# Optimization experiments

Measured on AMD Instinct MI355X. Metric: run time of the kernel, lower is better.

## Reference

```python
import jax, jax.numpy as jnp
import numpy as np

B, S, D, H, DFF = 2, 2048, 1024, 16, 4096
DH = D // H
EPS = 1e-5


def setup_inputs() -> dict:
    key = jax.random.key(0)
    ks = jax.random.split(key, 12)
    s = 0.02
    x = jax.random.normal(ks[0], (B, S, D), dtype=jnp.float32)
    # causal decoder mask, True = keep
    mask = jnp.tril(jnp.ones((S, S), dtype=bool))[None, None, :, :]
    Wq = jax.random.normal(ks[1], (D, D), dtype=jnp.float32) * s
    Wk = jax.random.normal(ks[2], (D, D), dtype=jnp.float32) * s
    Wv = jax.random.normal(ks[3], (D, D), dtype=jnp.float32) * s
    Wo = jax.random.normal(ks[4], (D, D), dtype=jnp.float32) * s
    w1 = jax.random.normal(ks[5], (D, DFF), dtype=jnp.float32) * s
    b1 = jnp.zeros((DFF,), dtype=jnp.float32)
    w2 = jax.random.normal(ks[6], (DFF, D), dtype=jnp.float32) * s
    b2 = jnp.zeros((D,), dtype=jnp.float32)
    g1 = jnp.ones((D,), dtype=jnp.float32)
    be1 = jnp.zeros((D,), dtype=jnp.float32)
    g2 = jnp.ones((D,), dtype=jnp.float32)
    be2 = jnp.zeros((D,), dtype=jnp.float32)
    return dict(x=x, mask=mask, Wq=Wq, Wk=Wk, Wv=Wv, Wo=Wo,
                w1=w1, b1=b1, w2=w2, b2=b2, g1=g1, be1=be1, g2=g2, be2=be2)


def _layer_norm(x, gamma, beta):
    mu = jnp.mean(x, axis=-1, keepdims=True)
    var = jnp.mean(jnp.square(x - mu), axis=-1, keepdims=True)
    return (x - mu) * jax.lax.rsqrt(var + EPS) * gamma + beta


def _attention(x, mask, Wq, Wk, Wv, Wo):
    # x: [B,S,D] -> q,k,v: [B,H,S,DH]
    def split_heads(t):
        return t.reshape(x.shape[0], x.shape[1], H, DH).transpose(0, 2, 1, 3)
    q = split_heads(x @ Wq)
    k = split_heads(x @ Wk)
    v = split_heads(x @ Wv)
    scores = jnp.einsum('bhqd,bhkd->bhqk', q, k) / jnp.sqrt(jnp.float32(DH))
    scores = jnp.where(mask, scores, jnp.float32(-1e9))
    probs = jax.nn.softmax(scores, axis=-1)
    out = jnp.einsum('bhqk,bhkd->bhqd', probs, v)  # [B,H,S,DH]
    out = out.transpose(0, 2, 1, 3).reshape(x.shape[0], x.shape[1], -1)
    return out @ Wo


def reference(x, mask, Wq, Wk, Wv, Wo, w1, b1, w2, b2, g1, be1, g2, be2):
    # residual 1: pre-norm self-attention (dropout=0)
    h = x + _attention(_layer_norm(x, g1, be1), mask, Wq, Wk, Wv, Wo)
    # residual 2: pre-norm FFN
    hn = _layer_norm(h, g2, be2)
    ffn = jax.nn.relu(hn @ w1 + b1) @ w2 + b2
    return h + ffn
```

## Files before the change

kernel.cpp:

```cpp
#include <hip/hip_runtime.h>

typedef unsigned short u16;
typedef __attribute__((ext_vector_type(8))) short short8;
typedef __attribute__((ext_vector_type(4))) float f32x4;

#define CB 2
#define CS 2048
#define CD 1024
#define CH 16
#define CDH 64
#define CDFF 4096
#define NQB (CS / 64)

__device__ __forceinline__ u16 f2bf(float f){
  union { float f; unsigned u; } x; x.f = f;
  unsigned r = (x.u + 0x7fffu + ((x.u >> 16) & 1u)) >> 16;
  return (u16)r;
}

__device__ __forceinline__ u16 f2bf_pos(float f){
  union { float f; unsigned u; } x; x.f = f;
  return (u16)((x.u + 0x8000u) >> 16);
}

__device__ __forceinline__ void gload_lds16(const void* g, void* l){
  __builtin_amdgcn_global_load_lds(
    (const __attribute__((address_space(1))) void*)(unsigned long long)g,
    (__attribute__((address_space(3))) void*)(unsigned long long)l,
    16, 0, 0);
}


struct TPAll { const float* s[6]; u16* d[6]; };

__global__ __launch_bounds__(256)
void prep_all(TPAll p, const float* __restrict__ x, const float* __restrict__ g1,
              const float* __restrict__ be1, u16* __restrict__ yln)
{
  const int g = blockIdx.x >> 12;
  const int id = blockIdx.x & 4095;
  const int tid = threadIdx.x;

  if (g == 3){
    const int row = id;
    const int lane = tid & 63, wave = tid >> 6;
    const float4 v = ((const float4*)(x + (size_t)row * CD))[tid];
    float s  = v.x + v.y + v.z + v.w;
    float s2 = v.x*v.x + v.y*v.y + v.z*v.z + v.w*v.w;
    #pragma unroll
    for (int m = 1; m < 64; m <<= 1){ s += __shfl_xor(s, m); s2 += __shfl_xor(s2, m); }
    __shared__ float red[8];
    if (lane == 0){ red[wave] = s; red[4 + wave] = s2; }
    __syncthreads();
    s  = red[0] + red[1] + red[2] + red[3];
    s2 = red[4] + red[5] + red[6] + red[7];
    const float mu = s * (1.0f / CD);
    const float var = s2 * (1.0f / CD) - mu * mu;
    const float rs = rsqrtf(var + 1e-5f);
    const float4 gv = ((const float4*)g1)[tid];
    const float4 bv = ((const float4*)be1)[tid];
    ushort4 o;
    o.x = f2bf((v.x - mu) * rs * gv.x + bv.x);
    o.y = f2bf((v.y - mu) * rs * gv.y + bv.y);
    o.z = f2bf((v.z - mu) * rs * gv.z + bv.z);
    o.w = f2bf((v.w - mu) * rs * gv.w + bv.w);
    ((ushort4*)yln)[(size_t)row * (CD / 4) + tid] = o;
    return;
  }

  __shared__ float t[32][33];
  const float* __restrict__ in;
  u16* __restrict__ out;
  int K, N, n0, k0;
  if (g == 0){
    const int w = id >> 10, tile = id & 1023;
    in = p.s[w]; out = p.d[w]; K = 1024; N = 1024;
    n0 = (tile & 31) * 32; k0 = (tile >> 5) * 32;
  } else if (g == 1){
    in = p.s[4]; out = p.d[4]; K = 1024; N = 4096;
    n0 = (id & 127) * 32; k0 = (id >> 7) * 32;
  } else {
    in = p.s[5]; out = p.d[5]; K = 4096; N = 1024;
    n0 = (id & 31) * 32; k0 = (id >> 5) * 32;
  }
  const int c = tid & 31, r4 = tid >> 5;
  #pragma unroll
  for (int i = 0; i < 4; i++){
    int r = r4 + i * 8;
    t[r][c] = in[(size_t)(k0 + r) * N + n0 + c];
  }
  __syncthreads();
  #pragma unroll
  for (int i = 0; i < 4; i++){
    int r = r4 + i * 8;
    out[(size_t)(n0 + r) * K + k0 + c] = f2bf(t[c][r]);
  }
}

template<int MODE>
__global__ __launch_bounds__(256)
void ln_bf16(const float* __restrict__ xin, const float* __restrict__ g,
             const float* __restrict__ be, u16* __restrict__ outp,
             float4* __restrict__ aux, const float* __restrict__ bias)
{
  const int row = blockIdx.x, tid = threadIdx.x;
  const int lane = tid & 63, wave = tid >> 6;
  const float4 v = ((const float4*)(xin + (size_t)row * CD))[tid];
  float s  = v.x + v.y + v.z + v.w;
  float s2 = v.x*v.x + v.y*v.y + v.z*v.z + v.w*v.w;
  #pragma unroll
  for (int m = 1; m < 64; m <<= 1){ s += __shfl_xor(s, m); s2 += __shfl_xor(s2, m); }
  __shared__ float red[8];
  if (lane == 0){ red[wave] = s; red[4 + wave] = s2; }

  if (MODE == 2){
    const float4 b4 = ((const float4*)bias)[tid];
    float4 w = v;
    w.x += b4.x; w.y += b4.y; w.z += b4.z; w.w += b4.w;
    aux[(size_t)row * 256 + tid] = w;
  }

  __syncthreads();
  s  = red[0] + red[1] + red[2] + red[3];
  s2 = red[4] + red[5] + red[6] + red[7];
  const float mu = s * (1.0f / CD);
  const float var = s2 * (1.0f / CD) - mu * mu;
  const float rs = rsqrtf(var + 1e-5f);
  const float4 gv = ((const float4*)g)[tid];
  const float4 bv = ((const float4*)be)[tid];
  ushort4 o;
  o.x = f2bf((v.x - mu) * rs * gv.x + bv.x);
  o.y = f2bf((v.y - mu) * rs * gv.y + bv.y);
  o.z = f2bf((v.z - mu) * rs * gv.z + bv.z);
  o.w = f2bf((v.w - mu) * rs * gv.w + bv.w);
  ((ushort4*)outp)[(size_t)row * (CD / 4) + tid] = o;
}

template<int EPI>
__global__ __launch_bounds__(512)
void gemm_bt(const u16* __restrict__ A, const u16* __restrict__ Bt,
             void* __restrict__ Cout, const float* __restrict__ bias,
             int M, int N, int K,
             int ldc, int vsplit, u16* __restrict__ vtout)
{
  __shared__ __align__(16) u16 sA[2][2][128 * 64];
  __shared__ __align__(16) u16 sB[2][2][128 * 64];
  const int tid = threadIdx.x;
  const int wave = tid >> 6, lane = tid & 63;
  const int wm = wave >> 2, wn = wave & 3;

  const int G = gridDim.x;
  const int flat = blockIdx.x;
  const int t0_ = (flat & 7) * (G >> 3) + (flat >> 3);
  const int NN = N >> 8;
  const int n_i = t0_ % NN;
  const int m_i = t0_ / NN;

  const int m0 = m_i * 256, n0 = n_i * 256;
  const int lq = lane >> 4, lr = lane & 15;
  const int l7 = lr & 7;
  const int sw0 = ((lq ^ l7) << 3);
  const int sw1 = (((4 + lq) ^ l7) << 3);

  f32x4 acc[8][4] = {};

  const u16* Ab = A + (size_t)m0 * K;
  const u16* Bb = Bt + (size_t)n0 * K;
  const int srow = lane >> 3;
  const int scol = (((lane & 7) ^ srow)) * 8;

  auto stageA = [&](int par, int h, int kt){
    const u16* src = Ab + (size_t)(h * 128) * K + kt * 64;
    u16* dst = &sA[par][h][0];
    #pragma unroll
    for (int i = 0; i < 2; i++){
      const int c = wave * 2 + i;
      gload_lds16(src + (size_t)(c * 8 + srow) * K + scol, dst + c * 512);
    }
  };
  auto stageB = [&](int par, int h, int kt){
    const u16* src = Bb + (size_t)(h * 128) * K + kt * 64;
    u16* dst = &sB[par][h][0];
    #pragma unroll
    for (int i = 0; i < 2; i++){
      const int c = wave * 2 + i;
      gload_lds16(src + (size_t)(c * 8 + srow) * K + scol, dst + c * 512);
    }
  };

  const int nt = K >> 6;

  stageB(0, 0, 0); stageB(0, 1, 0);
  stageA(0, 0, 0); stageA(0, 1, 0);
  stageB(1, 0, 1); stageB(1, 1, 1);
  asm volatile("s_waitcnt vmcnt(4)\n\ts_barrier" ::: "memory");

  short8 bF0[4], bF1[4];

  for (int t = 0; t < nt; t++){
    const int par = t & 1;
    const u16* aT = &sA[par][wm][0];
    const u16* bT = &sB[par][wn >> 1][0];
    const int bbase = (wn & 1) * 64;

    #pragma unroll
    for (int tq = 0; tq < 4; tq++){
      if (tq == 0){
        #pragma unroll
        for (int j = 0; j < 4; j++){
          bF0[j] = *(const short8*)&bT[(bbase + j * 16 + lr) * 64 + sw0];
          bF1[j] = *(const short8*)&bT[(bbase + j * 16 + lr) * 64 + sw1];
        }
      }
      const short8 a00 = *(const short8*)&aT[((tq * 2 + 0) * 16 + lr) * 64 + sw0];
      const short8 a01 = *(const short8*)&aT[((tq * 2 + 0) * 16 + lr) * 64 + sw1];
      const short8 a10 = *(const short8*)&aT[((tq * 2 + 1) * 16 + lr) * 64 + sw0];
      const short8 a11 = *(const short8*)&aT[((tq * 2 + 1) * 16 + lr) * 64 + sw1];

      if (tq == 0){ if (t + 1 < nt) stageA(par ^ 1, 0, t + 1); }
      if (tq == 1){ if (t + 1 < nt) stageA(par ^ 1, 1, t + 1); }
      if (tq == 2){ if (t + 2 < nt) stageB(par, 0, t + 2); }
      if (tq == 3){ if (t + 2 < nt) stageB(par, 1, t + 2); }

      asm volatile("s_barrier" ::: "memory");
      asm volatile("s_waitcnt lgkmcnt(0)" ::: "memory");
      __builtin_amdgcn_sched_barrier(0);

      __builtin_amdgcn_s_setprio(1);
      #pragma unroll
      for (int j = 0; j < 4; j++){
        acc[tq * 2 + 0][j] = __builtin_amdgcn_mfma_f32_16x16x32_bf16(a00, bF0[j], acc[tq * 2 + 0][j], 0, 0, 0);
        acc[tq * 2 + 0][j] = __builtin_amdgcn_mfma_f32_16x16x32_bf16(a01, bF1[j], acc[tq * 2 + 0][j], 0, 0, 0);
        acc[tq * 2 + 1][j] = __builtin_amdgcn_mfma_f32_16x16x32_bf16(a10, bF0[j], acc[tq * 2 + 1][j], 0, 0, 0);
        acc[tq * 2 + 1][j] = __builtin_amdgcn_mfma_f32_16x16x32_bf16(a11, bF1[j], acc[tq * 2 + 1][j], 0, 0, 0);
      }
      __builtin_amdgcn_s_setprio(0);

      if (tq == 3){
        if (t == nt - 2){
          asm volatile("s_waitcnt vmcnt(0)\n\ts_barrier" ::: "memory");
        } else if (t < nt - 2){
          asm volatile("s_waitcnt vmcnt(4)\n\ts_barrier" ::: "memory");
        } else {
          asm volatile("s_barrier" ::: "memory");
        }
      } else {
        asm volatile("s_barrier" ::: "memory");
      }
    }
  }

  if (EPI == 0 && n0 >= vsplit){
    #pragma unroll
    for (int mf = 0; mf < 8; mf++){
      const int row0 = m0 + wm * 128 + mf * 16 + lq * 4;
      const int bb = row0 >> 11, s = row0 & 2047;
      #pragma unroll
      for (int nf = 0; nf < 4; nf++){
        const int col = n0 - vsplit + wn * 64 + nf * 16 + lr;
        ushort4 o;
        o.x = f2bf(acc[mf][nf][0]); o.y = f2bf(acc[mf][nf][1]);
        o.z = f2bf(acc[mf][nf][2]); o.w = f2bf(acc[mf][nf][3]);
        *(ushort4*)&vtout[((size_t)(bb * 1024 + col)) * CS + s] = o;
      }
    }
    return;
  }

  const float osc = (EPI == 0 && n0 < 1024) ? 0.125f : 1.0f;

  #pragma unroll
  for (int mf = 0; mf < 8; mf++){
    const int row = m0 + wm * 128 + mf * 16 + lq * 4;
    #pragma unroll
    for (int nf = 0; nf < 4; nf++){
      const int col = n0 + wn * 64 + nf * 16 + lr;
      #pragma unroll
      for (int r = 0; r < 4; r++){
        float v = acc[mf][nf][r];
        const size_t off = (size_t)(row + r) * ldc + col;
        if (EPI == 0){
          ((u16*)Cout)[off] = f2bf(v * osc);
        } else {
          v += bias[col]; v = v > 0.0f ? v : 0.0f;
          ((u16*)Cout)[off] = f2bf(v);
        }
      }
    }
  }
}

__global__ __launch_bounds__(256)
void gemm_bt64(const u16* __restrict__ A, const u16* __restrict__ Bt,
               const float* __restrict__ resid, float* __restrict__ Cout,
               int M, int N, int K)
{
  __shared__ __align__(16) u16 lA[2][64 * 64];
  __shared__ __align__(16) u16 lB[2][128 * 64];
  const int tid = threadIdx.x;
  const int wave = tid >> 6, lane = tid & 63;

  const int G = gridDim.x;
  const int flat = blockIdx.x;
  const int t = (flat & 7) * (G >> 3) + (flat >> 3);
  const int NN = N >> 7;
  const int n_i = t % NN;
  const int m_i = t / NN;
  const int m0 = m_i * 64, n0 = n_i * 128;
  const int lq = lane >> 4, lr = lane & 15;
  const int l7 = lr & 7;
  const int sw0 = ((lq ^ l7) << 3);
  const int sw1 = (((4 + lq) ^ l7) << 3);

  f32x4 acc[4][2] = {};

  const u16* Ab = A + (size_t)m0 * K;
  const u16* Bb = Bt + (size_t)n0 * K;
  const int srow = lane >> 3;
  const int scol = (((lane & 7) ^ srow)) * 8;

  auto stage = [&](int buf, int kt){
    const int k0 = kt * 64;
    #pragma unroll
    for (int i = 0; i < 6; i++){
      const int c = i * 4 + wave;
      if (c < 8){
        gload_lds16(Ab + (size_t)(c * 8 + srow) * K + k0 + scol, &lA[buf][c * 512]);
      } else {
        const int cb2 = c - 8;
        gload_lds16(Bb + (size_t)(cb2 * 8 + srow) * K + k0 + scol, &lB[buf][cb2 * 512]);
      }
    }
  };

  const int nit = K >> 6;
  stage(0, 0);
  for (int i = 0; i < nit; i++){
    const int cb = i & 1;
    if (i + 1 < nit){
      stage(cb ^ 1, i + 1);
      asm volatile("s_waitcnt vmcnt(6)\n\ts_barrier" ::: "memory");
    } else {
      asm volatile("s_waitcnt vmcnt(0)\n\ts_barrier" ::: "memory");
    }
    #pragma unroll
    for (int kh = 0; kh < 2; kh++){
      const int sw = kh ? sw1 : sw0;
      short8 aF[4], bF[2];
      #pragma unroll
      for (int i2 = 0; i2 < 4; i2++) aF[i2] = *(const short8*)&lA[cb][(i2 * 16 + lr) * 64 + sw];
      #pragma unroll
      for (int j = 0; j < 2; j++) bF[j] = *(const short8*)&lB[cb][(wave * 32 + j * 16 + lr) * 64 + sw];
      #pragma unroll
      for (int i2 = 0; i2 < 4; i2++)
        #pragma unroll
        for (int j = 0; j < 2; j++)
          acc[i2][j] = __builtin_amdgcn_mfma_f32_16x16x32_bf16(aF[i2], bF[j], acc[i2][j], 0, 0, 0);
    }
    asm volatile("s_barrier" ::: "memory");
  }

  #pragma unroll
  for (int i = 0; i < 4; i++){
    const int row = m0 + i * 16 + lq * 4;
    #pragma unroll
    for (int j = 0; j < 2; j++){
      const int col = n0 + wave * 32 + j * 16 + lr;
      #pragma unroll
      for (int r = 0; r < 4; r++){
        const size_t off = (size_t)(row + r) * N + col;
        Cout[off] = resid[off] + acc[i][j][r];
      }
    }
  }
}

__global__ __launch_bounds__(256)
void attn_kernel(const u16* __restrict__ qk, const u16* __restrict__ vt,
                 u16* __restrict__ outp)
{
  __shared__ __align__(16) u16 lK[2][64 * 64];
  __shared__ __align__(16) u16 lVt[2][64 * 64];
  __shared__ __align__(16) u16 lP[4][16 * 72];
  const int tid = threadIdx.x, wave = tid >> 6, lane = tid & 63;
  const int lq = lane >> 4, lr = lane & 15;
  const int l7 = lr & 7;
  const int sw0 = ((lq ^ l7) << 3);
  const int sw1 = (((4 + lq) ^ l7) << 3);
  const int bh = blockIdx.x, b = bh >> 4, h = bh & 15;
  const int RS = 2048;
  const int srow = lane >> 3;
  const int scol = (((lane & 7) ^ srow)) * 8;

  const size_t kbase = (size_t)(b * CS) * RS + 1024 + h * CDH;
  const size_t vbase = (size_t)(bh * CDH) * CS;
  u16* lPw = lP[wave];

  auto stageKV = [&](int buf, int kt){
    #pragma unroll
    for (int cc = 0; cc < 2; cc++){
      const int c = wave * 2 + cc;
      gload_lds16(qk + kbase + (size_t)(kt * 64 + c * 8 + srow) * RS + scol, &lK[buf][c * 512]);
      gload_lds16(vt + vbase + (size_t)(c * 8 + srow) * CS + kt * 64 + scol, &lVt[buf][c * 512]);
    }
  };

  const int iq = (NQB - 1) - blockIdx.y;
  const int q0 = iq * 64;
  const int ktmax = iq + 1;

  const int qrow = b * CS + q0 + wave * 16 + lr;
  const u16* qp = qk + (size_t)qrow * RS + h * CDH;
  const short8 qf0 = *(const short8*)(qp + lq * 8);
  const short8 qf1 = *(const short8*)(qp + 32 + lq * 8);

  f32x4 o[4] = {};
  float lsum = 0.0f;
  const int qg = q0 + wave * 16 + lr;

  stageKV(0, 0);
  for (int kt = 0; kt < ktmax; ++kt){
    const int cb = kt & 1;
    if (kt + 1 < ktmax){
      stageKV(cb ^ 1, kt + 1);
      asm volatile("s_waitcnt vmcnt(4)\n\ts_barrier" ::: "memory");
    } else {
      asm volatile("s_waitcnt vmcnt(0)\n\ts_barrier" ::: "memory");
    }

    f32x4 s[4] = {};
    #pragma unroll
    for (int nb = 0; nb < 4; nb++){
      const short8 bk0 = *(const short8*)&lK[cb][(nb * 16 + lr) * 64 + sw0];
      const short8 bk1 = *(const short8*)&lK[cb][(nb * 16 + lr) * 64 + sw1];
      s[nb] = __builtin_amdgcn_mfma_f32_16x16x32_bf16(bk0, qf0, s[nb], 0, 0, 0);
      s[nb] = __builtin_amdgcn_mfma_f32_16x16x32_bf16(bk1, qf1, s[nb], 0, 0, 0);
    }

    const bool diag = (kt + 1) == ktmax;
    #pragma unroll
    for (int nb = 0; nb < 4; nb++){
      float e0 = __expf(s[nb][0]);
      float e1 = __expf(s[nb][1]);
      float e2 = __expf(s[nb][2]);
      float e3 = __expf(s[nb][3]);
      if (diag){
        const int kb = kt * 64 + nb * 16 + lq * 4;
        e0 = (kb     <= qg) ? e0 : 0.0f;
        e1 = (kb + 1 <= qg) ? e1 : 0.0f;
        e2 = (kb + 2 <= qg) ? e2 : 0.0f;
        e3 = (kb + 3 <= qg) ? e3 : 0.0f;
      }
      lsum += (e0 + e1) + (e2 + e3);
      ushort4 pw;
      pw.x = f2bf_pos(e0);
      pw.y = f2bf_pos(e1);
      pw.z = f2bf_pos(e2);
      pw.w = f2bf_pos(e3);
      *(ushort4*)&lPw[lr * 72 + nb * 16 + lq * 4] = pw;
    }

    asm volatile("s_waitcnt lgkmcnt(0)" ::: "memory");
    const short8 pf0 = *(const short8*)&lPw[lr * 72 + lq * 8];
    const short8 pf1 = *(const short8*)&lPw[lr * 72 + 32 + lq * 8];

    #pragma unroll
    for (int nb = 0; nb < 4; nb++){
      const short8 bv0 = *(const short8*)&lVt[cb][(nb * 16 + lr) * 64 + sw0];
      const short8 bv1 = *(const short8*)&lVt[cb][(nb * 16 + lr) * 64 + sw1];
      o[nb] = __builtin_amdgcn_mfma_f32_16x16x32_bf16(pf0, bv0, o[nb], 0, 0, 0);
      o[nb] = __builtin_amdgcn_mfma_f32_16x16x32_bf16(pf1, bv1, o[nb], 0, 0, 0);
    }
    asm volatile("s_barrier" ::: "memory");
  }

  float l = lsum;
  l += __shfl_xor(l, 16);
  l += __shfl_xor(l, 32);
  const float inv = __builtin_amdgcn_rcpf(l);

  #pragma unroll
  for (int r = 0; r < 4; r++){
    const float invr = __shfl(inv, lq * 4 + r);
    const size_t row = (size_t)(b * CS + q0 + wave * 16 + lq * 4 + r);
    #pragma unroll
    for (int nb = 0; nb < 4; nb++)
      outp[row * CD + h * CDH + nb * 16 + lr] = f2bf(o[nb][r] * invr);
  }
}

extern "C" void kernel_launch(void* const* d_in, const int* in_sizes, int n_in,
                              void* d_out, int out_size, void* d_ws, size_t ws_size,
                              hipStream_t stream)
{
  const float* x   = (const float*)d_in[0];
  const float* Wq  = (const float*)d_in[2];
  const float* Wk  = (const float*)d_in[3];
  const float* Wv  = (const float*)d_in[4];
  const float* Wo  = (const float*)d_in[5];
  const float* w1  = (const float*)d_in[6];
  const float* b1  = (const float*)d_in[7];
  const float* w2  = (const float*)d_in[8];
  const float* b2  = (const float*)d_in[9];
  const float* g1  = (const float*)d_in[10];
  const float* be1 = (const float*)d_in[11];
  const float* g2  = (const float*)d_in[12];
  const float* be2 = (const float*)d_in[13];
  float* out = (float*)d_out;

  char* ws = (char*)d_ws;
  const size_t MB = 1u << 20;
  u16* yln    = (u16*)(ws);
  u16* qk     = (u16*)(ws + 8  * MB);
  u16* vt     = (u16*)(ws + 24 * MB);
  u16* attn   = (u16*)(ws + 32 * MB);
  u16* mid    = (u16*)(ws + 40 * MB);
  u16* Wqkv_t = (u16*)(ws + 72 * MB);
  u16* Wo_t   = (u16*)(ws + 78 * MB);
  u16* w1_t   = (u16*)(ws + 80 * MB);
  u16* w2_t   = (u16*)(ws + 88 * MB);

  const int M = CB * CS;
  const int BIG = 1 << 30;

  TPAll pa;
  pa.s[0] = Wq; pa.s[1] = Wk; pa.s[2] = Wv; pa.s[3] = Wo; pa.s[4] = w1; pa.s[5] = w2;
  pa.d[0] = Wqkv_t;
  pa.d[1] = Wqkv_t + (size_t)CD * CD;
  pa.d[2] = Wqkv_t + (size_t)2 * CD * CD;
  pa.d[3] = Wo_t;
  pa.d[4] = w1_t;
  pa.d[5] = w2_t;
  prep_all<<<4 * 4096, 256, 0, stream>>>(pa, x, g1, be1, yln);

  gemm_bt<0><<<192, 512, 0, stream>>>(yln, Wqkv_t, qk, nullptr, M, 3 * CD, CD, 2048, 2048, vt);
  attn_kernel<<<dim3(CB * CH, NQB), 256, 0, stream>>>(qk, vt, attn);
  gemm_bt64<<<64 * 8, 256, 0, stream>>>(attn, Wo_t, x, out, M, CD, CD);
  ln_bf16<2><<<M, 256, 0, stream>>>(out, g2, be2, yln, (float4*)out, b2);
  gemm_bt<1><<<256, 512, 0, stream>>>(yln, w1_t, mid, b1, M, CDFF, CD, CDFF, BIG, nullptr);
  gemm_bt64<<<64 * 8, 256, 0, stream>>>(mid, w2_t, out, out, M, CD, CDFF);
}
```

Baseline: 308.3 us.

## Split K across wave pairs in gemm_bt64 with LDS partial-sum reduction

After: 313.1 us. Within noise of the previous version (+1.6%).

```diff
diff --git a/kernel.cpp b/kernel.cpp
--- a/kernel.cpp
+++ b/kernel.cpp
@@ -309,10 +309,10 @@
   const int m0 = m_i * 64, n0 = n_i * 128;
   const int lq = lane >> 4, lr = lane & 15;
   const int l7 = lr & 7;
-  const int sw0 = ((lq ^ l7) << 3);
-  const int sw1 = (((4 + lq) ^ l7) << 3);
-
-  f32x4 acc[4][2] = {};
+  const int wn2 = wave & 1, wk = wave >> 1;
+  const int swK = ((wk * 4 + lq) ^ l7) << 3;
+
+  f32x4 acc[4][4] = {};
 
   const u16* Ab = A + (size_t)m0 * K;
   const u16* Bb = Bt + (size_t)n0 * K;
@@ -343,33 +343,70 @@
     } else {
       asm volatile("s_waitcnt vmcnt(0)\n\ts_barrier" ::: "memory");
     }
-    #pragma unroll
-    for (int kh = 0; kh < 2; kh++){
-      const int sw = kh ? sw1 : sw0;
-      short8 aF[4], bF[2];
+    short8 aF[4], bF[4];
+    #pragma unroll
+    for (int i2 = 0; i2 < 4; i2++) aF[i2] = *(const short8*)&lA[cb][(i2 * 16 + lr) * 64 + swK];
+    #pragma unroll
+    for (int j = 0; j < 4; j++) bF[j] = *(const short8*)&lB[cb][(wn2 * 64 + j * 16 + lr) * 64 + swK];
+    #pragma unroll
+    for (int i2 = 0; i2 < 4; i2++)
       #pragma unroll
-      for (int i2 = 0; i2 < 4; i2++) aF[i2] = *(const short8*)&lA[cb][(i2 * 16 + lr) * 64 + sw];
-      #pragma unroll
-      for (int j = 0; j < 2; j++) bF[j] = *(const short8*)&lB[cb][(wave * 32 + j * 16 + lr) * 64 + sw];
-      #pragma unroll
-      for (int i2 = 0; i2 < 4; i2++)
-        #pragma unroll
-        for (int j = 0; j < 2; j++)
-          acc[i2][j] = __builtin_amdgcn_mfma_f32_16x16x32_bf16(aF[i2], bF[j], acc[i2][j], 0, 0, 0);
-    }
+      for (int j = 0; j < 4; j++)
+        acc[i2][j] = __builtin_amdgcn_mfma_f32_16x16x32_bf16(aF[i2], bF[j], acc[i2][j], 0, 0, 0);
     asm volatile("s_barrier" ::: "memory");
   }
 
-  #pragma unroll
-  for (int i = 0; i < 4; i++){
-    const int row = m0 + i * 16 + lq * 4;
-    #pragma unroll
-    for (int j = 0; j < 2; j++){
-      const int col = n0 + wave * 32 + j * 16 + lr;
+  float* xch = (float*)&lB[0][0];
+  if (wk == 0){
+    #pragma unroll
+    for (int j = 0; j < 4; j++){
+      *(f32x4*)&xch[(((wn2 * 2 + 1) * 8) + 0 + j) * 256 + lane * 4] = acc[2][j];
+      *(f32x4*)&xch[(((wn2 * 2 + 1) * 8) + 4 + j) * 256 + lane * 4] = acc[3][j];
+    }
+  } else {
+    #pragma unroll
+    for (int j = 0; j < 4; j++){
+      *(f32x4*)&xch[(((wn2 * 2 + 0) * 8) + 0 + j) * 256 + lane * 4] = acc[0][j];
+      *(f32x4*)&xch[(((wn2 * 2 + 0) * 8) + 4 + j) * 256 + lane * 4] = acc[1][j];
+    }
+  }
+  __syncthreads();
+  if (wk == 0){
+    #pragma unroll
+    for (int j = 0; j < 4; j++){
+      const f32x4 p0 = *(const f32x4*)&xch[(((wn2 * 2 + 0) * 8) + 0 + j) * 256 + lane * 4];
+      const f32x4 p1 = *(const f32x4*)&xch[(((wn2 * 2 + 0) * 8) + 4 + j) * 256 + lane * 4];
+      acc[0][j] = acc[0][j] + p0;
+      acc[1][j] = acc[1][j] + p1;
+    }
+    #pragma unroll
+    for (int j = 0; j < 4; j++){
+      const int col = n0 + wn2 * 64 + j * 16 + lr;
       #pragma unroll
       for (int r = 0; r < 4; r++){
-        const size_t off = (size_t)(row + r) * N + col;
-        Cout[off] = resid[off] + acc[i][j][r];
+        const size_t off0 = (size_t)(m0 +  0 + lq * 4 + r) * N + col;
+        const size_t off1 = (size_t)(m0 + 16 + lq * 4 + r) * N + col;
+        Cout[off0] = resid[off0] + acc[0][j][r];
+        Cout[off1] = resid[off1] + acc[1][j][r];
+      }
+    }
+  } else {
+    #pragma unroll
+    for (int j = 0; j < 4; j++){
+      const f32x4 p0 = *(const f32x4*)&xch[(((wn2 * 2 + 1) * 8) + 0 + j) * 256 + lane * 4];
+      const f32x4 p1 = *(const f32x4*)&xch[(((wn2 * 2 + 1) * 8) + 4 + j) * 256 + lane * 4];
+      acc[2][j] = acc[2][j] + p0;
+      acc[3][j] = acc[3][j] + p1;
+    }
+    #pragma unroll
+    for (int j = 0; j < 4; j++){
+      const int col = n0 + wn2 * 64 + j * 16 + lr;
+      #pragma unroll
+      for (int r = 0; r < 4; r++){
+        const size_t off0 = (size_t)(m0 + 32 + lq * 4 + r) * N + col;
+        const size_t off1 = (size_t)(m0 + 48 + lq * 4 + r) * N + col;
+        Cout[off0] = resid[off0] + acc[2][j][r];
+        Cout[off1] = resid[off1] + acc[3][j][r];
       }
     }
   }
```
